# Kernel tuning notes

Hardware: AMD Instinct MI355X
Metric: run time of the kernel (lower is better)

Reference implementation:

```python
import jax, jax.numpy as jnp
import numpy as np

B, T, C = 2, 2048, 2048
NH, NKV, D = 16, 4, 128
N_REP = NH // NKV
THETA = 10000.0


def setup_inputs() -> dict:
    key = jax.random.key(0)
    ks = jax.random.split(key, 5)
    s = 0.02
    return {
        "x": jax.random.normal(ks[0], (B, T, C), dtype=jnp.float32),
        "Wq": jax.random.normal(ks[1], (C, C), dtype=jnp.float32) * s,
        "Wk": jax.random.normal(ks[2], (NKV * D, C), dtype=jnp.float32) * s,
        "Wv": jax.random.normal(ks[3], (NKV * D, C), dtype=jnp.float32) * s,
        "Wo": jax.random.normal(ks[4], (C, C), dtype=jnp.float32) * s,
    }


def _rope(t):
    # t: (B, H, T, D); rotate pairs (even, odd) by angle pos * theta_i
    inv_freq = 1.0 / (THETA ** (jnp.arange(0, D, 2, dtype=jnp.float32) / D))  # (D/2,)
    ang = jnp.arange(T, dtype=jnp.float32)[:, None] * inv_freq[None, :]       # (T, D/2)
    cos, sin = jnp.cos(ang), jnp.sin(ang)
    te, to = t[..., 0::2], t[..., 1::2]
    re = te * cos - to * sin
    ro = te * sin + to * cos
    return jnp.stack([re, ro], axis=-1).reshape(t.shape).astype(t.dtype)


def reference(x, Wq, Wk, Wv, Wo):
    # Projections (Linear: y = x @ W.T)
    q = (x @ Wq.T).reshape(B, T, NH, D).transpose(0, 2, 1, 3)    # (B,NH,T,D)
    k = (x @ Wk.T).reshape(B, T, NKV, D).transpose(0, 2, 1, 3)   # (B,NKV,T,D)
    v = (x @ Wv.T).reshape(B, T, NKV, D).transpose(0, 2, 1, 3)
    q = _rope(q)
    k = _rope(k)
    # GQA: group query heads per kv head instead of materializing repeated K/V
    qg = q.reshape(B, NKV, N_REP, T, D)                          # (B,G,R,T,D)
    scale = 1.0 / jnp.sqrt(jnp.float32(D))
    scores = jnp.einsum("bgrtd,bgsd->bgrts", qg, k) * scale      # (B,G,R,T,T)
    causal = jnp.tril(jnp.ones((T, T), dtype=bool))
    scores = jnp.where(causal, scores, jnp.finfo(scores.dtype).min)
    attn = jax.nn.softmax(scores, axis=-1)
    out = jnp.einsum("bgrts,bgsd->bgrtd", attn, v)               # (B,G,R,T,D)
    out = out.reshape(B, NH, T, D).transpose(0, 2, 1, 3).reshape(B, T, C)
    return out @ Wo.T
```

## Files before the change

kernel.cpp:

```cpp
#include <hip/hip_runtime.h>
#include <hip/hip_bf16.h>
#include <stdint.h>

#define B_   2
#define T_   2048
#define C_   2048
#define NH_  16
#define NKV_ 4
#define D_   128
#define NREP_ 4

typedef __attribute__((ext_vector_type(8))) short bf16x8;
typedef __attribute__((ext_vector_type(4))) float f32x4;

__device__ inline short f2bs(float f) {
    __hip_bfloat16 h = __float2bfloat16(f);
    return *reinterpret_cast<short*>(&h);
}
__device__ inline float bs2f(unsigned short s) {
    __hip_bfloat16 h = *reinterpret_cast<__hip_bfloat16*>(&s);
    return __bfloat162float(h);
}

__device__ inline void gl_lds16(const __hip_bfloat16* g, __hip_bfloat16* l) {
    __builtin_amdgcn_global_load_lds(
        (const __attribute__((address_space(1))) unsigned int*)g,
        (__attribute__((address_space(3))) unsigned int*)l,
        16, 0, 0);
}

__global__ void cvt_f32_bf16(const float* __restrict__ src,
                             __hip_bfloat16* __restrict__ dst, int n) {
    int i = (blockIdx.x * blockDim.x + threadIdx.x) * 4;
    if (i >= n) return;
    float4 v = *reinterpret_cast<const float4*>(src + i);
    short4 o;
    o.x = f2bs(v.x); o.y = f2bs(v.y); o.z = f2bs(v.z); o.w = f2bs(v.w);
    *reinterpret_cast<short4*>(dst + i) = o;
}

__device__ inline void storeC(float* p, float v) { *p = v; }
__device__ inline void storeC(__hip_bfloat16* p, float v) { *p = __float2bfloat16(v); }

template <typename OutT>
__global__ __launch_bounds__(256) void gemm_bt(const __hip_bfloat16* __restrict__ A,
                                               const __hip_bfloat16* __restrict__ Bm,
                                               OutT* __restrict__ Cm,
                                               int M, int N, int K) {
    __shared__ __hip_bfloat16 As[128 * 32];
    __shared__ __hip_bfloat16 Bs[128 * 32];
    const int tid  = threadIdx.x;
    const int lane = tid & 63;
    const int wv   = tid >> 6;
    const int m0 = blockIdx.y * 128, n0 = blockIdx.x * 128;
    const int wm = (wv >> 1) * 64, wn = (wv & 1) * 64;
    const int q16 = lane >> 4, r16 = lane & 15;

    f32x4 acc[4][4] = {};

    const int lrow = tid >> 2;
    const int lcol = (tid & 3) * 8;
    const __hip_bfloat16* aG = A  + (size_t)(m0 + lrow) * K + lcol;
    const __hip_bfloat16* bG = Bm + (size_t)(n0 + lrow) * K + lcol;
    __hip_bfloat16* aL = As + tid * 8;
    __hip_bfloat16* bL = Bs + tid * 8;

    for (int k0 = 0; k0 < K; k0 += 32) {
        __syncthreads();
        gl_lds16(aG + k0,          aL);
        gl_lds16(aG + 64 * K + k0, aL + 2048);
        gl_lds16(bG + k0,          bL);
        gl_lds16(bG + 64 * K + k0, bL + 2048);
        __syncthreads();
        bf16x8 af[4], bfr[4];
#pragma unroll
        for (int i = 0; i < 4; i++)
            af[i] = *reinterpret_cast<const bf16x8*>(As + (wm + i * 16 + r16) * 32 + q16 * 8);
#pragma unroll
        for (int j = 0; j < 4; j++)
            bfr[j] = *reinterpret_cast<const bf16x8*>(Bs + (wn + j * 16 + r16) * 32 + q16 * 8);
#pragma unroll
        for (int i = 0; i < 4; i++)
#pragma unroll
            for (int j = 0; j < 4; j++)
                acc[i][j] = __builtin_amdgcn_mfma_f32_16x16x32_bf16(af[i], bfr[j], acc[i][j], 0, 0, 0);
    }

#pragma unroll
    for (int i = 0; i < 4; i++)
#pragma unroll
        for (int j = 0; j < 4; j++)
#pragma unroll
            for (int r = 0; r < 4; r++) {
                int row = m0 + wm + i * 16 + q16 * 4 + r;
                int col = n0 + wn + j * 16 + r16;
                storeC(&Cm[(size_t)row * N + col], acc[i][j][r]);
            }
}

__global__ void rope_scatter(const __hip_bfloat16* __restrict__ y,
                             __hip_bfloat16* __restrict__ qo,
                             __hip_bfloat16* __restrict__ ko,
                             __hip_bfloat16* __restrict__ vT) {
    int idx = blockIdx.x * blockDim.x + threadIdx.x;
    if (idx >= (B_ * T_) * 1536) return;
    int m = idx / 1536, pc = idx % 1536;
    int b = m / T_, t = m % T_;
    int n = pc * 2;
    ushort2 uv = *reinterpret_cast<const ushort2*>(y + (size_t)m * 3072 + n);
    float e = bs2f(uv.x), od = bs2f(uv.y);

    if (n < 2560) {
        int nn = (n < 2048) ? n : (n - 2048);
        int dloc = nn & 127;
        int p = dloc >> 1;
        float inv = __expf(-(float)p * (9.210340371976184f / 64.0f));
        float ang = (float)t * inv;
        float c = cosf(ang), s = sinf(ang);
        float re = e * c - od * s;
        float ro = e * s + od * c;
        ushort2 w;
        w.x = (unsigned short)f2bs(re);
        w.y = (unsigned short)f2bs(ro);
        if (n < 2048) {
            int h = n >> 7;
            *reinterpret_cast<ushort2*>(qo + ((size_t)(b * NH_ + h) * T_ + t) * D_ + dloc) = w;
        } else {
            int h = nn >> 7;
            *reinterpret_cast<ushort2*>(ko + ((size_t)(b * NKV_ + h) * T_ + t) * D_ + dloc) = w;
        }
    } else {
        int nn = n - 2560;
        int h = nn >> 7, d = nn & 127;
        __hip_bfloat16* base = vT + (size_t)(b * NKV_ + h) * D_ * T_;
        base[(size_t)d * T_ + t]       = __float2bfloat16(e);
        base[(size_t)(d + 1) * T_ + t] = __float2bfloat16(od);
    }
}

__global__ __launch_bounds__(256, 3) void attn_kernel(const __hip_bfloat16* __restrict__ Q,
                                                      const __hip_bfloat16* __restrict__ Kt,
                                                      const __hip_bfloat16* __restrict__ Vt,
                                                      __hip_bfloat16* __restrict__ Ao,
                                                      float* __restrict__ O0,
                                                      float* __restrict__ O1,
                                                      float* __restrict__ l0p,
                                                      float* __restrict__ l1p) {
    __shared__ __hip_bfloat16 Ks[2][4096];
    __shared__ __hip_bfloat16 Vs[2][4096];
    __shared__ __hip_bfloat16 Pl[4][1280];

    const int lane = threadIdx.x & 63, wv = threadIdx.x >> 6;
    const int bg = blockIdx.y;
    const int u  = (int)blockIdx.x;
    int tb, nIt, sIdx;
    if (u < 32)      { tb = u;      nIt = tb + 1;      sIdx = -1; }
    else if (u < 64) { tb = u;      nIt = 32;          sIdx = 0;  }
    else             { tb = u - 32; nIt = tb + 1 - 32; sIdx = 1;  }
    const int sBase = (sIdx == 1) ? 1024 : 0;
    const int b = bg >> 2, g = bg & 3;
    const int h = g * 4 + wv;
    const int t0 = tb * 32;
    const int q16 = lane >> 4, r16 = lane & 15;

    const __hip_bfloat16* qh = Q + ((size_t)((b * NH_ + h) * T_) + t0) * D_;
    const __hip_bfloat16* kh = Kt + (size_t)(b * NKV_ + g) * T_ * D_;
    const __hip_bfloat16* vh = Vt + (size_t)(b * NKV_ + g) * D_ * T_;

    bf16x8 bqA[4], bqB[4];
#pragma unroll
    for (int kk = 0; kk < 4; kk++) {
        bqA[kk] = *reinterpret_cast<const bf16x8*>(qh + (size_t)r16 * D_ + kk * 32 + q16 * 8);
        bqB[kk] = *reinterpret_cast<const bf16x8*>(qh + (size_t)(16 + r16) * D_ + kk * 32 + q16 * 8);
    }

    float liA = 0.f, liB = 0.f;
    f32x4 oA[8], oB[8];
#pragma unroll
    for (int d = 0; d < 8; d++) {
        oA[d] = (f32x4){0.f, 0.f, 0.f, 0.f};
        oB[d] = (f32x4){0.f, 0.f, 0.f, 0.f};
    }

    const float SCL2 = 0.088388347648318447f * 1.4426950408889634f;
    const int tqA = t0 + r16;
    const int tqB = t0 + 16 + r16;

    const __hip_bfloat16* gK = kh + (size_t)((wv & 1) * 16 + r16) * D_ + q16 * 8;
    const __hip_bfloat16* gV = vh + (size_t)(((wv - 2) * 4) * 16 + r16) * T_ + q16 * 8;

#define STAGE(bufi, s0_)                                                        \
    do {                                                                        \
        if (wv < 2) {                                                           \
            const __hip_bfloat16* gp = gK + (size_t)(s0_) * D_;                 \
            __hip_bfloat16* lp = &Ks[bufi][(wv * 4) * 512] + lane * 8;          \
            gl_lds16(gp,      lp);                                              \
            gl_lds16(gp + 32, lp + 512);                                        \
            gl_lds16(gp + 64, lp + 1024);                                       \
            gl_lds16(gp + 96, lp + 1536);                                       \
        } else {                                                                \
            const __hip_bfloat16* gp = gV + (s0_);                              \
            __hip_bfloat16* lp = &Vs[bufi][((wv - 2) * 4) * 512] + lane * 8;    \
            gl_lds16(gp,                      lp);                              \
            gl_lds16(gp + (size_t)16 * T_,    lp + 512);                        \
            gl_lds16(gp + (size_t)32 * T_,    lp + 1024);                       \
            gl_lds16(gp + (size_t)48 * T_,    lp + 1536);                       \
        }                                                                       \
    } while (0)

    STAGE(0, sBase);

    for (int j = 0; j < nIt; j++) {
        const int s0 = sBase + j * 32;
        const int cur = j & 1;
        __syncthreads();
        if (j + 1 < nIt) STAGE(cur ^ 1, s0 + 32);

        f32x4 sc0A = (f32x4){0.f, 0.f, 0.f, 0.f};
        f32x4 sc1A = (f32x4){0.f, 0.f, 0.f, 0.f};
        f32x4 sc0B = (f32x4){0.f, 0.f, 0.f, 0.f};
        f32x4 sc1B = (f32x4){0.f, 0.f, 0.f, 0.f};
        {
            bf16x8 ak[4];
#pragma unroll
            for (int kk = 0; kk < 4; kk++)
                ak[kk] = *reinterpret_cast<const bf16x8*>(&Ks[cur][kk * 512] + lane * 8);
#pragma unroll
            for (int kk = 0; kk < 4; kk++) {
                sc0A = __builtin_amdgcn_mfma_f32_16x16x32_bf16(ak[kk], bqA[kk], sc0A, 0, 0, 0);
                sc0B = __builtin_amdgcn_mfma_f32_16x16x32_bf16(ak[kk], bqB[kk], sc0B, 0, 0, 0);
            }
#pragma unroll
            for (int kk = 0; kk < 4; kk++)
                ak[kk] = *reinterpret_cast<const bf16x8*>(&Ks[cur][(4 + kk) * 512] + lane * 8);
#pragma unroll
            for (int kk = 0; kk < 4; kk++) {
                sc1A = __builtin_amdgcn_mfma_f32_16x16x32_bf16(ak[kk], bqA[kk], sc1A, 0, 0, 0);
                sc1B = __builtin_amdgcn_mfma_f32_16x16x32_bf16(ak[kk], bqB[kk], sc1B, 0, 0, 0);
            }
        }

        ushort4 w0A, w1A, w0B, w1B;
        float psA = 0.f, psB = 0.f;
        if (s0 + 32 > t0) {
#pragma unroll
            for (int r = 0; r < 4; r++) {
                int s_a = s0 + q16 * 4 + r;
                float pa0 = (s_a <= tqA)      ? __builtin_amdgcn_exp2f(sc0A[r] * SCL2) : 0.f;
                float pa1 = (s_a + 16 <= tqA) ? __builtin_amdgcn_exp2f(sc1A[r] * SCL2) : 0.f;
                float pb0 = (s_a <= tqB)      ? __builtin_amdgcn_exp2f(sc0B[r] * SCL2) : 0.f;
                float pb1 = (s_a + 16 <= tqB) ? __builtin_amdgcn_exp2f(sc1B[r] * SCL2) : 0.f;
                psA += pa0 + pa1;
                psB += pb0 + pb1;
                ((unsigned short*)&w0A)[r] = (unsigned short)f2bs(pa0);
                ((unsigned short*)&w1A)[r] = (unsigned short)f2bs(pa1);
                ((unsigned short*)&w0B)[r] = (unsigned short)f2bs(pb0);
                ((unsigned short*)&w1B)[r] = (unsigned short)f2bs(pb1);
            }
        } else {
#pragma unroll
            for (int r = 0; r < 4; r++) {
                float pa0 = __builtin_amdgcn_exp2f(sc0A[r] * SCL2);
                float pa1 = __builtin_amdgcn_exp2f(sc1A[r] * SCL2);
                float pb0 = __builtin_amdgcn_exp2f(sc0B[r] * SCL2);
                float pb1 = __builtin_amdgcn_exp2f(sc1B[r] * SCL2);
                psA += pa0 + pa1;
                psB += pb0 + pb1;
                ((unsigned short*)&w0A)[r] = (unsigned short)f2bs(pa0);
                ((unsigned short*)&w1A)[r] = (unsigned short)f2bs(pa1);
                ((unsigned short*)&w0B)[r] = (unsigned short)f2bs(pb0);
                ((unsigned short*)&w1B)[r] = (unsigned short)f2bs(pb1);
            }
        }
        liA += psA;
        liB += psB;

        *reinterpret_cast<ushort4*>(&Pl[wv][r16 * 40 + q16 * 4]) = w0A;
        *reinterpret_cast<ushort4*>(&Pl[wv][r16 * 40 + 16 + q16 * 4]) = w1A;
        *reinterpret_cast<ushort4*>(&Pl[wv][640 + r16 * 40 + q16 * 4]) = w0B;
        *reinterpret_cast<ushort4*>(&Pl[wv][640 + r16 * 40 + 16 + q16 * 4]) = w1B;
        asm volatile("s_waitcnt lgkmcnt(0)" ::: "memory");
        bf16x8 pfA = *reinterpret_cast<const bf16x8*>(&Pl[wv][r16 * 40 + q16 * 8]);
        bf16x8 pfB = *reinterpret_cast<const bf16x8*>(&Pl[wv][640 + r16 * 40 + q16 * 8]);

#pragma unroll
        for (int d = 0; d < 8; d++) {
            bf16x8 bv = *reinterpret_cast<const bf16x8*>(&Vs[cur][d * 512] + lane * 8);
            oA[d] = __builtin_amdgcn_mfma_f32_16x16x32_bf16(pfA, bv, oA[d], 0, 0, 0);
            oB[d] = __builtin_amdgcn_mfma_f32_16x16x32_bf16(pfB, bv, oB[d], 0, 0, 0);
        }
    }

    liA += __shfl_xor(liA, 16);
    liA += __shfl_xor(liA, 32);
    liB += __shfl_xor(liB, 16);
    liB += __shfl_xor(liB, 32);

    if (sIdx < 0) {
#pragma unroll
        for (int r = 0; r < 4; r++) {
            float lrA = __shfl(liA, q16 * 4 + r, 16);
            float lrB = __shfl(liB, q16 * 4 + r, 16);
            float invA = 1.0f / lrA;
            float invB = 1.0f / lrB;
            int tA = t0 + q16 * 4 + r;
            __hip_bfloat16* dstA = Ao + (size_t)(b * T_ + tA) * C_ + h * D_ + r16;
            __hip_bfloat16* dstB = dstA + (size_t)16 * C_;
#pragma unroll
            for (int d = 0; d < 8; d++) {
                dstA[d * 16] = __float2bfloat16(oA[d][r] * invA);
                dstB[d * 16] = __float2bfloat16(oB[d][r] * invB);
            }
        }
    } else {
        float* Os = (sIdx == 0) ? O0 : O1;
        float* ls = (sIdx == 0) ? l0p : l1p;
        const size_t rb = (size_t)(b * NH_ + h) * 1024 + (size_t)(t0 - 1024);
        if (q16 == 0) {
            ls[rb + r16]      = liA;
            ls[rb + 16 + r16] = liB;
        }
#pragma unroll
        for (int r = 0; r < 4; r++) {
            int rowl = q16 * 4 + r;
            float* dA = Os + (rb + rowl) * 128 + r16;
            float* dB = Os + (rb + 16 + rowl) * 128 + r16;
#pragma unroll
            for (int d = 0; d < 8; d++) {
                dA[d * 16] = oA[d][r];
                dB[d * 16] = oB[d][r];
            }
        }
    }
#undef STAGE
}

__global__ void attn_combine(const float* __restrict__ O0, const float* __restrict__ O1,
                             const float* __restrict__ l0, const float* __restrict__ l1,
                             __hip_bfloat16* __restrict__ Ao) {
    int idx = blockIdx.x * blockDim.x + threadIdx.x;
    int row = idx >> 5, d4 = (idx & 31) << 2;
    int bh = row >> 10, tl = row & 1023;
    int b = bh >> 4, h = bh & 15;
    float inv = 1.0f / (l0[row] + l1[row]);
    float4 a = *reinterpret_cast<const float4*>(O0 + (size_t)row * 128 + d4);
    float4 c = *reinterpret_cast<const float4*>(O1 + (size_t)row * 128 + d4);
    short4 o;
    o.x = f2bs((a.x + c.x) * inv);
    o.y = f2bs((a.y + c.y) * inv);
    o.z = f2bs((a.z + c.z) * inv);
    o.w = f2bs((a.w + c.w) * inv);
    *reinterpret_cast<short4*>(Ao + (size_t)(b * T_ + 1024 + tl) * C_ + h * D_ + d4) = o;
}

extern "C" void kernel_launch(void* const* d_in, const int* in_sizes, int n_in,
                              void* d_out, int out_size, void* d_ws, size_t ws_size,
                              hipStream_t stream) {
    const float* x  = (const float*)d_in[0];
    const float* Wq = (const float*)d_in[1];
    const float* Wk = (const float*)d_in[2];
    const float* Wv = (const float*)d_in[3];
    const float* Wo = (const float*)d_in[4];
    float* out = (float*)d_out;
    char* ws = (char*)d_ws;

    __hip_bfloat16* xb   = (__hip_bfloat16*)(ws + 0);
    __hip_bfloat16* wcat = (__hip_bfloat16*)(ws + 16777216);
    __hip_bfloat16* wob  = (__hip_bfloat16*)(ws + 29360128);
    __hip_bfloat16* yq   = (__hip_bfloat16*)(ws + 37748736);
    __hip_bfloat16* qatt = (__hip_bfloat16*)(ws + 62914560);
    __hip_bfloat16* katt = (__hip_bfloat16*)(ws + 79691776);
    __hip_bfloat16* vT   = (__hip_bfloat16*)(ws + 83886080);
    __hip_bfloat16* aout = (__hip_bfloat16*)(ws + 88080384);

    float* O0 = (float*)(ws + 0);
    float* O1 = (float*)(ws + 37748736);
    float* l0 = (float*)(ws + 37748736 + 16777216);
    float* l1 = (float*)(ws + 37748736 + 16777216 + 131072);

    const int thr = 256;
    cvt_f32_bf16<<<(B_ * T_ * C_ / 4 + thr - 1) / thr, thr, 0, stream>>>(x, xb, B_ * T_ * C_);
    cvt_f32_bf16<<<(C_ * C_ / 4 + thr - 1) / thr, thr, 0, stream>>>(Wq, wcat, C_ * C_);
    cvt_f32_bf16<<<(512 * 2048 / 4 + thr - 1) / thr, thr, 0, stream>>>(Wk, wcat + C_ * C_, 512 * 2048);
    cvt_f32_bf16<<<(512 * 2048 / 4 + thr - 1) / thr, thr, 0, stream>>>(Wv, wcat + C_ * C_ + 512 * 2048, 512 * 2048);
    cvt_f32_bf16<<<(C_ * C_ / 4 + thr - 1) / thr, thr, 0, stream>>>(Wo, wob, C_ * C_);

    gemm_bt<__hip_bfloat16><<<dim3(24, 32), 256, 0, stream>>>(xb, wcat, yq, 4096, 3072, 2048);

    rope_scatter<<<(B_ * T_ * 1536 + thr - 1) / thr, thr, 0, stream>>>(yq, qatt, katt, vT);

    attn_kernel<<<dim3(96, 8), 256, 0, stream>>>(qatt, katt, vT, aout, O0, O1, l0, l1);
    attn_combine<<<(2 * NH_ * 1024 * 32) / thr, thr, 0, stream>>>(O0, O1, l0, l1, aout);

    gemm_bt<float><<<dim3(16, 32), 256, 0, stream>>>(aout, wob, out, 4096, 2048, 2048);
}
```

Baseline: 330.6 us.

## Fuse RoPE and QKV scatter into projection GEMM epilogue, merge conversion kernels

The five f32-to-bf16 conversion launches are merged into one prep kernel, which also builds a precomputed cos/sin RoPE table. The QKV projection GEMM now applies RoPE in its epilogue, getting each pair partner with a lane shuffle, and writes Q, K and transposed V directly. This removes the intermediate yq buffer round trip and the separate rope_scatter kernel. The cost is strided bf16 scalar stores from the GEMM epilogue, especially for the transposed V, plus table lookups.

```diff
diff --git a/kernel.cpp b/kernel.cpp
--- a/kernel.cpp
+++ b/kernel.cpp
@@ -17,10 +17,6 @@
     __hip_bfloat16 h = __float2bfloat16(f);
     return *reinterpret_cast<short*>(&h);
 }
-__device__ inline float bs2f(unsigned short s) {
-    __hip_bfloat16 h = *reinterpret_cast<__hip_bfloat16*>(&s);
-    return __bfloat162float(h);
-}
 
 __device__ inline void gl_lds16(const __hip_bfloat16* g, __hip_bfloat16* l) {
     __builtin_amdgcn_global_load_lds(
@@ -29,14 +25,36 @@
         16, 0, 0);
 }
 
-__global__ void cvt_f32_bf16(const float* __restrict__ src,
-                             __hip_bfloat16* __restrict__ dst, int n) {
-    int i = (blockIdx.x * blockDim.x + threadIdx.x) * 4;
-    if (i >= n) return;
-    float4 v = *reinterpret_cast<const float4*>(src + i);
-    short4 o;
-    o.x = f2bs(v.x); o.y = f2bs(v.y); o.z = f2bs(v.z); o.w = f2bs(v.w);
-    *reinterpret_cast<short4*>(dst + i) = o;
+__global__ void prep_kernel(const float* __restrict__ x,  const float* __restrict__ Wq,
+                            const float* __restrict__ Wk, const float* __restrict__ Wv,
+                            const float* __restrict__ Wo,
+                            __hip_bfloat16* __restrict__ xb, __hip_bfloat16* __restrict__ wcat,
+                            __hip_bfloat16* __restrict__ wob, float2* __restrict__ ropeTab) {
+    int tid = blockIdx.x * blockDim.x + threadIdx.x;
+    const int CVT_THREADS = 4718592;
+    if (tid < CVT_THREADS) {
+        int i4 = tid * 4;
+        const float* src;
+        __hip_bfloat16* dst;
+        int off;
+        if (i4 < 8388608)       { src = x;  dst = xb;             off = i4; }
+        else if (i4 < 12582912) { src = Wq; dst = wcat;           off = i4 - 8388608; }
+        else if (i4 < 13631488) { src = Wk; dst = wcat + 4194304; off = i4 - 12582912; }
+        else if (i4 < 14680064) { src = Wv; dst = wcat + 5242880; off = i4 - 13631488; }
+        else                    { src = Wo; dst = wob;            off = i4 - 14680064; }
+        float4 v = *reinterpret_cast<const float4*>(src + off);
+        short4 o;
+        o.x = f2bs(v.x); o.y = f2bs(v.y); o.z = f2bs(v.z); o.w = f2bs(v.w);
+        *reinterpret_cast<short4*>(dst + off) = o;
+    } else {
+        int e = tid - CVT_THREADS;
+        if (e < 131072) {
+            int t = e >> 6, p = e & 63;
+            float inv = __expf(-(float)p * (9.210340371976184f / 64.0f));
+            float ang = (float)t * inv;
+            ropeTab[e] = make_float2(cosf(ang), sinf(ang));
+        }
+    }
 }
 
 __device__ inline void storeC(float* p, float v) { *p = v; }
@@ -98,44 +116,83 @@
             }
 }
 
-__global__ void rope_scatter(const __hip_bfloat16* __restrict__ y,
-                             __hip_bfloat16* __restrict__ qo,
-                             __hip_bfloat16* __restrict__ ko,
-                             __hip_bfloat16* __restrict__ vT) {
-    int idx = blockIdx.x * blockDim.x + threadIdx.x;
-    if (idx >= (B_ * T_) * 1536) return;
-    int m = idx / 1536, pc = idx % 1536;
-    int b = m / T_, t = m % T_;
-    int n = pc * 2;
-    ushort2 uv = *reinterpret_cast<const ushort2*>(y + (size_t)m * 3072 + n);
-    float e = bs2f(uv.x), od = bs2f(uv.y);
-
-    if (n < 2560) {
-        int nn = (n < 2048) ? n : (n - 2048);
-        int dloc = nn & 127;
-        int p = dloc >> 1;
-        float inv = __expf(-(float)p * (9.210340371976184f / 64.0f));
-        float ang = (float)t * inv;
-        float c = cosf(ang), s = sinf(ang);
-        float re = e * c - od * s;
-        float ro = e * s + od * c;
-        ushort2 w;
-        w.x = (unsigned short)f2bs(re);
-        w.y = (unsigned short)f2bs(ro);
-        if (n < 2048) {
-            int h = n >> 7;
-            *reinterpret_cast<ushort2*>(qo + ((size_t)(b * NH_ + h) * T_ + t) * D_ + dloc) = w;
-        } else {
-            int h = nn >> 7;
-            *reinterpret_cast<ushort2*>(ko + ((size_t)(b * NKV_ + h) * T_ + t) * D_ + dloc) = w;
-        }
-    } else {
-        int nn = n - 2560;
-        int h = nn >> 7, d = nn & 127;
-        __hip_bfloat16* base = vT + (size_t)(b * NKV_ + h) * D_ * T_;
-        base[(size_t)d * T_ + t]       = __float2bfloat16(e);
-        base[(size_t)(d + 1) * T_ + t] = __float2bfloat16(od);
-    }
+__global__ __launch_bounds__(256) void gemm_qkv(const __hip_bfloat16* __restrict__ A,
+                                                const __hip_bfloat16* __restrict__ Bm,
+                                                const float2* __restrict__ ropeTab,
+                                                __hip_bfloat16* __restrict__ qo,
+                                                __hip_bfloat16* __restrict__ ko,
+                                                __hip_bfloat16* __restrict__ vT) {
+    const int K = 2048;
+    __shared__ __hip_bfloat16 As[128 * 32];
+    __shared__ __hip_bfloat16 Bs[128 * 32];
+    const int tid  = threadIdx.x;
+    const int lane = tid & 63;
+    const int wv   = tid >> 6;
+    const int m0 = blockIdx.y * 128, n0 = blockIdx.x * 128;
+    const int wm = (wv >> 1) * 64, wn = (wv & 1) * 64;
+    const int q16 = lane >> 4, r16 = lane & 15;
+
+    f32x4 acc[4][4] = {};
+
+    const int lrow = tid >> 2;
+    const int lcol = (tid & 3) * 8;
+    const __hip_bfloat16* aG = A  + (size_t)(m0 + lrow) * K + lcol;
+    const __hip_bfloat16* bG = Bm + (size_t)(n0 + lrow) * K + lcol;
+    __hip_bfloat16* aL = As + tid * 8;
+    __hip_bfloat16* bL = Bs + tid * 8;
+
+    for (int k0 = 0; k0 < K; k0 += 32) {
+        __syncthreads();
+        gl_lds16(aG + k0,          aL);
+        gl_lds16(aG + 64 * K + k0, aL + 2048);
+        gl_lds16(bG + k0,          bL);
+        gl_lds16(bG + 64 * K + k0, bL + 2048);
+        __syncthreads();
+        bf16x8 af[4], bfr[4];
+#pragma unroll
+        for (int i = 0; i < 4; i++)
+            af[i] = *reinterpret_cast<const bf16x8*>(As + (wm + i * 16 + r16) * 32 + q16 * 8);
+#pragma unroll
+        for (int j = 0; j < 4; j++)
+            bfr[j] = *reinterpret_cast<const bf16x8*>(Bs + (wn + j * 16 + r16) * 32 + q16 * 8);
+#pragma unroll
+        for (int i = 0; i < 4; i++)
+#pragma unroll
+            for (int j = 0; j < 4; j++)
+                acc[i][j] = __builtin_amdgcn_mfma_f32_16x16x32_bf16(af[i], bfr[j], acc[i][j], 0, 0, 0);
+    }
+
+    const int hb = n0 >> 7;
+    const float sgn = (r16 & 1) ? 1.0f : -1.0f;
+#pragma unroll
+    for (int i = 0; i < 4; i++)
+#pragma unroll
+        for (int r = 0; r < 4; r++) {
+            const int m = m0 + wm + i * 16 + q16 * 4 + r;
+            const int b = m >> 11, t = m & 2047;
+            if (hb < 20) {
+                const float2* tabRow = ropeTab + t * 64;
+                __hip_bfloat16* dst = (hb < 16)
+                    ? qo + ((size_t)(b * NH_ + hb) * T_ + t) * D_
+                    : ko + ((size_t)(b * NKV_ + (hb - 16)) * T_ + t) * D_;
+#pragma unroll
+                for (int j = 0; j < 4; j++) {
+                    const int dloc = wn + j * 16 + r16;
+                    float v = acc[i][j][r];
+                    float prt = __shfl_xor(v, 1);
+                    float2 cs = tabRow[dloc >> 1];
+                    float res = fmaf(prt * sgn, cs.y, v * cs.x);
+                    dst[dloc] = __float2bfloat16(res);
+                }
+            } else {
+                __hip_bfloat16* dst = vT + (size_t)(b * NKV_ + (hb - 20)) * D_ * T_ + t;
+#pragma unroll
+                for (int j = 0; j < 4; j++) {
+                    const int d = wn + j * 16 + r16;
+                    dst[(size_t)d * T_] = __float2bfloat16(acc[i][j][r]);
+                }
+            }
+        }
 }
 
 __global__ __launch_bounds__(256, 3) void attn_kernel(const __hip_bfloat16* __restrict__ Q,
@@ -197,7 +254,7 @@
             gl_lds16(gp,      lp);                                              \
             gl_lds16(gp + 32, lp + 512);                                        \
             gl_lds16(gp + 64, lp + 1024);                                       \
-            gl_lds16(gp + 96, lp + 1536);                                       \
+            gl_lds16(gp + 96, lp + 1536);                                      \
         } else {                                                                \
             const __hip_bfloat16* gp = gV + (s0_);                              \
             __hip_bfloat16* lp = &Vs[bufi][((wv - 2) * 4) * 512] + lane * 8;    \
@@ -366,28 +423,21 @@
 
     __hip_bfloat16* xb   = (__hip_bfloat16*)(ws + 0);
     __hip_bfloat16* wcat = (__hip_bfloat16*)(ws + 16777216);
-    __hip_bfloat16* wob  = (__hip_bfloat16*)(ws + 29360128);
-    __hip_bfloat16* yq   = (__hip_bfloat16*)(ws + 37748736);
-    __hip_bfloat16* qatt = (__hip_bfloat16*)(ws + 62914560);
-    __hip_bfloat16* katt = (__hip_bfloat16*)(ws + 79691776);
-    __hip_bfloat16* vT   = (__hip_bfloat16*)(ws + 83886080);
-    __hip_bfloat16* aout = (__hip_bfloat16*)(ws + 88080384);
-
+    float2*         ropeTab = (float2*)(ws + 29360128);
+    __hip_bfloat16* wob  = (__hip_bfloat16*)(ws + 30408704);
+    __hip_bfloat16* qatt = (__hip_bfloat16*)(ws + 38797312);
+    __hip_bfloat16* katt = (__hip_bfloat16*)(ws + 55574528);
+    __hip_bfloat16* vT   = (__hip_bfloat16*)(ws + 59768832);
+    __hip_bfloat16* aout = (__hip_bfloat16*)(ws + 63963136);
     float* O0 = (float*)(ws + 0);
-    float* O1 = (float*)(ws + 37748736);
-    float* l0 = (float*)(ws + 37748736 + 16777216);
-    float* l1 = (float*)(ws + 37748736 + 16777216 + 131072);
+    float* O1 = (float*)(ws + 80740352);
+    float* l0 = (float*)(ws + 97517568);
+    float* l1 = (float*)(ws + 97648640);
 
     const int thr = 256;
-    cvt_f32_bf16<<<(B_ * T_ * C_ / 4 + thr - 1) / thr, thr, 0, stream>>>(x, xb, B_ * T_ * C_);
-    cvt_f32_bf16<<<(C_ * C_ / 4 + thr - 1) / thr, thr, 0, stream>>>(Wq, wcat, C_ * C_);
-    cvt_f32_bf16<<<(512 * 2048 / 4 + thr - 1) / thr, thr, 0, stream>>>(Wk, wcat + C_ * C_, 512 * 2048);
-    cvt_f32_bf16<<<(512 * 2048 / 4 + thr - 1) / thr, thr, 0, stream>>>(Wv, wcat + C_ * C_ + 512 * 2048, 512 * 2048);
-    cvt_f32_bf16<<<(C_ * C_ / 4 + thr - 1) / thr, thr, 0, stream>>>(Wo, wob, C_ * C_);
-
-    gemm_bt<__hip_bfloat16><<<dim3(24, 32), 256, 0, stream>>>(xb, wcat, yq, 4096, 3072, 2048);
-
-    rope_scatter<<<(B_ * T_ * 1536 + thr - 1) / thr, thr, 0, stream>>>(yq, qatt, katt, vT);
+    prep_kernel<<<18944, thr, 0, stream>>>(x, Wq, Wk, Wv, Wo, xb, wcat, wob, ropeTab);
+
+    gemm_qkv<<<dim3(24, 32), 256, 0, stream>>>(xb, wcat, ropeTab, qatt, katt, vT);
 
     attn_kernel<<<dim3(96, 8), 256, 0, stream>>>(qatt, katt, vT, aout, O0, O1, l0, l1);
     attn_combine<<<(2 * NH_ * 1024 * 32) / thr, thr, 0, stream>>>(O0, O1, l0, l1, aout);
```

After: 304.6 us. -7.9%, faster.
